# Kernel optimization log

Hardware: AMD Instinct MI355X
Metric: run time of the kernel (lower is better)

## Reference

```python
import jax, jax.numpy as jnp
import numpy as np

B, C, H, W = 8, 512, 64, 64
NH, D = 8, 64            # num_heads, head_dim (C = NH*D)
WH, WW = 8, 8            # window size
EPS = 1e-5
SCALE = D ** -0.5


def _layernorm(x, g, b):
    mu = jnp.mean(x, axis=-1, keepdims=True)
    var = jnp.mean((x - mu) ** 2, axis=-1, keepdims=True)
    return (x - mu) * jax.lax.rsqrt(var + EPS) * g + b


def _rope_cache(n, d):
    pos = jnp.arange(n, dtype=jnp.float32)
    inv_freq = 1.0 / (10000.0 ** (jnp.arange(0, d, 2, dtype=jnp.float32) / d))
    sinusoid = pos[:, None] * inv_freq[None, :]          # (n, d//2)
    return jnp.stack([jnp.sin(sinusoid), jnp.cos(sinusoid)], axis=-1).reshape(n, d)


def _apply_rope(x, rope):
    # x: (B, nH, N, d); rope: (N, d) packed [sin, cos] interleaved
    b, nh, n, d = x.shape
    x_ = x.reshape(b, nh, n, d // 2, 2)
    r = rope.reshape(n, d // 2, 2)
    sin, cos = r[..., 0], r[..., 1]                      # (N, d//2)
    x0, x1 = x_[..., 0], x_[..., 1]
    xr0 = x0 * cos - x1 * sin
    xr1 = x0 * sin + x1 * cos
    return jnp.stack([xr0, xr1], axis=-1).reshape(b, nh, n, d)


def _relative_index(wh, ww):
    ch, cw = np.meshgrid(np.arange(wh), np.arange(ww), indexing='ij')
    flat = np.stack([ch.reshape(-1), cw.reshape(-1)])    # (2, Ws)
    rel = flat[:, :, None] - flat[:, None, :]            # (2, Ws, Ws)
    rel = rel.transpose(1, 2, 0).astype(np.int64)
    rel[..., 0] += wh - 1
    rel[..., 1] += ww - 1
    rel[..., 0] *= 2 * ww - 1
    return jnp.asarray(rel.sum(-1))                      # (Ws, Ws)


def setup_inputs() -> dict:
    key = jax.random.key(0)
    ks = jax.random.split(key, 12)
    s = 0.02
    table_size = (2 * WH - 1) * (2 * WW - 1)
    return {
        'q':  jax.random.normal(ks[0], (B, C, H, W), jnp.float32),
        'kv': jax.random.normal(ks[1], (B, C, H, W), jnp.float32),
        'g_q':  jnp.ones((C,), jnp.float32),  'b_q_ln':  jnp.zeros((C,), jnp.float32),
        'g_kv': jnp.ones((C,), jnp.float32),  'b_kv_ln': jnp.zeros((C,), jnp.float32),
        'Wq': jax.random.normal(ks[2], (C, C), jnp.float32) * s, 'bq': jnp.zeros((C,), jnp.float32),
        'Wk': jax.random.normal(ks[3], (C, C), jnp.float32) * s, 'bk': jnp.zeros((C,), jnp.float32),
        'Wv': jax.random.normal(ks[4], (C, C), jnp.float32) * s, 'bv': jnp.zeros((C,), jnp.float32),
        'Wo': jax.random.normal(ks[5], (C, C), jnp.float32) * s, 'bo': jnp.zeros((C,), jnp.float32),
        'bias_table': jax.random.normal(ks[6], (table_size, NH), jnp.float32) * s,
    }


def reference(q, kv, g_q, b_q_ln, g_kv, b_kv_ln, Wq, bq, Wk, bk, Wv, bv, Wo, bo, bias_table):
    N = H * W
    Hn, Wn = H // WH, W // WW
    nw = Hn * Wn
    Ws = WH * WW

    # flatten NCHW -> (B, N, C)
    q_seq = q.reshape(B, C, N).transpose(0, 2, 1)
    kv_seq = kv.reshape(B, C, N).transpose(0, 2, 1)
    q_seq = _layernorm(q_seq, g_q, b_q_ln)
    kv_seq = _layernorm(kv_seq, g_kv, b_kv_ln)

    Q = (q_seq @ Wq.T + bq).reshape(B, N, NH, D).transpose(0, 2, 1, 3)   # (B,nH,N,d)
    K = (kv_seq @ Wk.T + bk).reshape(B, N, NH, D).transpose(0, 2, 1, 3)
    V = (kv_seq @ Wv.T + bv).reshape(B, N, NH, D).transpose(0, 2, 1, 3)

    rope = _rope_cache(N, D)
    Q = _apply_rope(Q, rope)
    K = _apply_rope(K, rope)

    # window partition: (B,nH,H,W,d) -> (nH, B*nw, Ws, d); head-major to match torch cat order
    def part(x):
        x = x.reshape(B, NH, Hn, WH, Wn, WW, D)
        return x.transpose(1, 0, 2, 4, 3, 5, 6).reshape(NH, B * nw, Ws, D)

    Qw, Kw, Vw = part(Q), part(K), part(V)

    attn = jnp.einsum('hnqd,hnkd->hnqk', Qw, Kw) * SCALE                 # (nH, B*nw, Ws, Ws)
    rel_idx = _relative_index(WH, WW)
    bias = bias_table[rel_idx.reshape(-1)].reshape(Ws, Ws, NH).transpose(2, 0, 1)  # (nH, Ws, Ws)
    attn = attn + bias[:, None, :, :]
    attn = jax.nn.softmax(attn, axis=-1)
    out_w = jnp.einsum('hnqk,hnkd->hnqd', attn, Vw)                      # (nH, B*nw, Ws, d)

    # window reverse + head concat -> (B, N, C)
    out = out_w.reshape(NH, B, Hn, Wn, WH, WW, D)
    out = out.transpose(1, 2, 4, 3, 5, 0, 6).reshape(B, N, NH * D)

    out = out @ Wo.T + bo
    out = out + q_seq                                                    # residual w/ normed q (as in source)
    return out.transpose(0, 2, 1).reshape(B, C, H, W)
```

## Files before the change

### kernel.cpp

```cpp
#include <hip/hip_runtime.h>


typedef unsigned short u16;
typedef __bf16 bf16x8 __attribute__((ext_vector_type(8)));
typedef float f32x4 __attribute__((ext_vector_type(4)));
typedef u16 u16x8 __attribute__((ext_vector_type(8)));

__device__ __forceinline__ u16 f2bf(float f) {
    __bf16 h = (__bf16)f;
    return __builtin_bit_cast(u16, h);
}
__device__ __forceinline__ float bf2f(u16 u) {
    return (float)__builtin_bit_cast(__bf16, u);
}
__device__ __forceinline__ f32x4 mfma16(bf16x8 a, bf16x8 b, f32x4 c) {
    return __builtin_amdgcn_mfma_f32_16x16x32_bf16(a, b, c, 0, 0, 0);
}

__global__ __launch_bounds__(256) void setup_kernel(
    const float* __restrict__ Wq, const float* __restrict__ Wk,
    const float* __restrict__ Wv, const float* __restrict__ Wo,
    const float* __restrict__ btab,
    u16* __restrict__ wq, u16* __restrict__ wk,
    u16* __restrict__ wv, u16* __restrict__ wo,
    float* __restrict__ rope, float* __restrict__ biasf)
{
    int idx = blockIdx.x * 256 + threadIdx.x;
    {
        int w = idx >> 18, e = idx & 262143;
        const float* src = (w == 0) ? Wq : (w == 1) ? Wk : (w == 2) ? Wv : Wo;
        u16* dst = (w == 0) ? wq : (w == 1) ? wk : (w == 2) ? wv : wo;
        dst[e] = f2bf(src[e]);
    }
    if (idx < 131072) {
        int n = idx >> 5, j = idx & 31;
        float inv = powf(10000.0f, -(float)j / 32.0f);
        float a = (float)n * inv;
        float s, c;
        sincosf(a, &s, &c);
        rope[n * 64 + 2 * j] = s;
        rope[n * 64 + 2 * j + 1] = c;
    }
    if (idx < 32768) {
        int q = idx & 63, pp = (idx >> 6) & 63, h = idx >> 12;
        int r1 = pp >> 3, c1 = pp & 7, r2 = q >> 3, c2 = q & 7;
        int ri = (r1 - r2 + 7) * 15 + (c1 - c2 + 7);
        biasf[idx] = btab[ri * 8 + h];
    }
}

__global__ __launch_bounds__(256) void ln_kernel(
    const float* __restrict__ x, const float* __restrict__ g,
    const float* __restrict__ be, u16* __restrict__ out)
{
    __shared__ u16 sX[512 * 36];
    __shared__ float sSum[256];
    __shared__ float sSq[256];
    __shared__ float sMu[32], sInv[32];

    const int tid = threadIdx.x;
    const int b = blockIdx.x >> 7, grp = blockIdx.x & 127;
    const int nbase = grp << 5;
    const int no = tid & 31, cg = tid >> 5;

    const float* xp = x + ((size_t)b << 21) + nbase + no;
    float sum = 0.f, sq = 0.f;
#pragma unroll 4
    for (int i = 0; i < 64; i++) {
        int c = (i << 3) + cg;
        float v = xp[(size_t)c << 12];
        sum += v;
        sq += v * v;
        sX[c * 36 + no] = f2bf(v);
    }
    sSum[tid] = sum;
    sSq[tid] = sq;
    __syncthreads();
    if (tid < 32) {
        float s = 0.f, q = 0.f;
#pragma unroll
        for (int k = 0; k < 8; k++) { s += sSum[k * 32 + tid]; q += sSq[k * 32 + tid]; }
        float mu = s * (1.f / 512.f);
        float var = q * (1.f / 512.f) - mu * mu;
        sMu[tid] = mu;
        sInv[tid] = rsqrtf(var + 1e-5f);
    }
    __syncthreads();

    const int t = tid & 31;
    const int chalf = (tid >> 5) << 3;
    float mu = sMu[t], inv = sInv[t];
    size_t orow = ((size_t)((b << 12) + nbase + t)) * 512;
#pragma unroll
    for (int it = 0; it < 8; it++) {
        int c0 = chalf + (it << 6);
        f32x4 g0 = *(const f32x4*)&g[c0];
        f32x4 g1 = *(const f32x4*)&g[c0 + 4];
        f32x4 e0 = *(const f32x4*)&be[c0];
        f32x4 e1 = *(const f32x4*)&be[c0 + 4];
        u16x8 o;
#pragma unroll
        for (int k = 0; k < 8; k++) {
            float v = bf2f(sX[(c0 + k) * 36 + t]);
            float gg = (k < 4) ? g0[k] : g1[k - 4];
            float bb = (k < 4) ? e0[k] : e1[k - 4];
            o[k] = f2bf((v - mu) * inv * gg + bb);
        }
        *(u16x8*)&out[orow + c0] = o;
    }
}

template <bool ROPE>
__global__ __launch_bounds__(256) void gemm_proj(
    const u16* __restrict__ A, const u16* __restrict__ Bw,
    const float* __restrict__ bias, const float* __restrict__ rope,
    u16* __restrict__ Out)
{
    __shared__ u16 sA[128 * 40];
    __shared__ u16 sB[128 * 40];
    __shared__ u16 sC[64 * 136];

    const int m0 = blockIdx.x * 128;
    const int n0 = blockIdx.y * 128;
    const int tid = threadIdx.x;
    const int lane = tid & 63, wave = tid >> 6;
    const int ln = lane & 15, lq = lane >> 4;
    const int wm = wave & 1, wn = wave >> 1;

    f32x4 acc[4][4] = {};

    for (int kt = 0; kt < 512; kt += 32) {
        __syncthreads();
#pragma unroll
        for (int ps = 0; ps < 2; ps++) {
            int idx = (ps << 8) + tid;
            int row = idx >> 2, seg = idx & 3;
            *(u16x8*)&sA[row * 40 + seg * 8] =
                *(const u16x8*)&A[(size_t)(m0 + row) * 512 + kt + seg * 8];
            *(u16x8*)&sB[row * 40 + seg * 8] =
                *(const u16x8*)&Bw[(size_t)(n0 + row) * 512 + kt + seg * 8];
        }
        __syncthreads();
        bf16x8 af[4], bfr[4];
#pragma unroll
        for (int i = 0; i < 4; i++)
            af[i] = *(const bf16x8*)&sA[(wm * 64 + i * 16 + ln) * 40 + lq * 8];
#pragma unroll
        for (int j = 0; j < 4; j++)
            bfr[j] = *(const bf16x8*)&sB[(wn * 64 + j * 16 + ln) * 40 + lq * 8];
#pragma unroll
        for (int i = 0; i < 4; i++)
#pragma unroll
            for (int j = 0; j < 4; j++)
                acc[i][j] = mfma16(af[i], bfr[j], acc[i][j]);
    }

    float bj[4];
#pragma unroll
    for (int j = 0; j < 4; j++) bj[j] = bias[n0 + wn * 64 + j * 16 + ln];

#pragma unroll
    for (int half = 0; half < 2; half++) {
        __syncthreads();
        if (wm == half) {
#pragma unroll
            for (int i = 0; i < 4; i++)
#pragma unroll
                for (int j = 0; j < 4; j++)
#pragma unroll
                    for (int r = 0; r < 4; r++)
                        sC[(i * 16 + lq * 4 + r) * 136 + wn * 64 + j * 16 + ln] =
                            f2bf(acc[i][j][r] + bj[j]);
        }
        __syncthreads();
#pragma unroll
        for (int it = 0; it < 4; it++) {
            int idx = it * 256 + tid;
            int row = idx >> 4;
            int cseg = (idx & 15) * 8;
            u16x8 v = *(const u16x8*)&sC[row * 136 + cseg];
            int t = m0 + half * 64 + row;
            float f[8];
#pragma unroll
            for (int k = 0; k < 8; k++) f[k] = bf2f(v[k]);
            if (ROPE) {
                int n = t & 4095;
                int d0 = cseg & 63;
                const float* rp = &rope[n * 64 + d0];
                f32x4 r0 = *(const f32x4*)rp;
                f32x4 r1 = *(const f32x4*)(rp + 4);
#pragma unroll
                for (int p = 0; p < 4; p++) {
                    float sn = (p < 2) ? r0[2 * p] : r1[2 * (p - 2)];
                    float cs = (p < 2) ? r0[2 * p + 1] : r1[2 * (p - 2) + 1];
                    float x0 = f[2 * p], x1 = f[2 * p + 1];
                    f[2 * p] = x0 * cs - x1 * sn;
                    f[2 * p + 1] = x0 * sn + x1 * cs;
                }
            }
            u16x8 o;
#pragma unroll
            for (int k = 0; k < 8; k++) o[k] = f2bf(f[k]);
            *(u16x8*)&Out[(size_t)t * 512 + n0 + cseg] = o;
        }
    }
}

__global__ __launch_bounds__(256) void gemm_out(
    const u16* __restrict__ A, const u16* __restrict__ Bw,
    const float* __restrict__ bias, const u16* __restrict__ qn,
    float* __restrict__ Out)
{
    __shared__ u16 sA[128 * 40];
    __shared__ u16 sB[128 * 40];

    const int m0 = blockIdx.x * 128;
    const int n0 = blockIdx.y * 128;
    const int tid = threadIdx.x;
    const int lane = tid & 63, wave = tid >> 6;
    const int ln = lane & 15, lq = lane >> 4;
    const int wm = wave & 1, wn = wave >> 1;

    f32x4 acc[4][4] = {};

    for (int kt = 0; kt < 512; kt += 32) {
        __syncthreads();
#pragma unroll
        for (int ps = 0; ps < 2; ps++) {
            int idx = (ps << 8) + tid;
            int row = idx >> 2, seg = idx & 3;
            *(u16x8*)&sA[row * 40 + seg * 8] =
                *(const u16x8*)&A[(size_t)(m0 + row) * 512 + kt + seg * 8];
            *(u16x8*)&sB[row * 40 + seg * 8] =
                *(const u16x8*)&Bw[(size_t)(n0 + row) * 512 + kt + seg * 8];
        }
        __syncthreads();
        bf16x8 af[4], bfr[4];
#pragma unroll
        for (int i = 0; i < 4; i++)
            af[i] = *(const bf16x8*)&sA[(wm * 64 + i * 16 + ln) * 40 + lq * 8];
#pragma unroll
        for (int j = 0; j < 4; j++)
            bfr[j] = *(const bf16x8*)&sB[(wn * 64 + j * 16 + ln) * 40 + lq * 8];
#pragma unroll
        for (int i = 0; i < 4; i++)
#pragma unroll
            for (int j = 0; j < 4; j++)
                acc[i][j] = mfma16(af[i], bfr[j], acc[i][j]);
    }

    int cj[4];
    float bj[4];
#pragma unroll
    for (int j = 0; j < 4; j++) {
        cj[j] = n0 + wn * 64 + j * 16 + ln;
        bj[j] = bias[cj[j]];
    }
#pragma unroll
    for (int i = 0; i < 4; i++) {
        int t0 = m0 + wm * 64 + i * 16 + lq * 4;
        int bb = t0 >> 12, nn = t0 & 4095;
#pragma unroll
        for (int j = 0; j < 4; j++) {
            f32x4 v;
#pragma unroll
            for (int r = 0; r < 4; r++)
                v[r] = acc[i][j][r] + bj[j] + bf2f(qn[(size_t)(t0 + r) * 512 + cj[j]]);
            *(f32x4*)&Out[((size_t)((bb << 9) + cj[j]) << 12) + nn] = v;
        }
    }
}

__global__ __launch_bounds__(256) void attn_kernel(
    const u16* __restrict__ Q, const u16* __restrict__ K, const u16* __restrict__ V,
    const float* __restrict__ biasf, u16* __restrict__ Out)
{
    __shared__ u16 sQ[64 * 72];
    __shared__ u16 sK[64 * 72];
    __shared__ u16 sVT[64 * 72];
    __shared__ u16 sP[4][16 * 72];

    const int tid = threadIdx.x;
    const int h = blockIdx.x & 7;
    const int g = blockIdx.x >> 3;
    const int b = g >> 6, wi = g & 63;
    const int hn = wi >> 3, wn = wi & 7;
    const int nwbase = (b << 12) + (hn << 3) * 64 + (wn << 3);

    const int lane = tid & 63, wave = tid >> 6;
    const int ln = lane & 15, lq = lane >> 4;

    {
        int p = tid >> 2, seg = tid & 3;
        int t = nwbase + ((p >> 3) << 6) + (p & 7);
        size_t base = (size_t)t * 512 + h * 64 + seg * 16;
        u16x8 q0 = *(const u16x8*)&Q[base];
        u16x8 q1 = *(const u16x8*)&Q[base + 8];
        *(u16x8*)&sQ[p * 72 + seg * 16] = q0;
        *(u16x8*)&sQ[p * 72 + seg * 16 + 8] = q1;
        u16x8 k0 = *(const u16x8*)&K[base];
        u16x8 k1 = *(const u16x8*)&K[base + 8];
        *(u16x8*)&sK[p * 72 + seg * 16] = k0;
        *(u16x8*)&sK[p * 72 + seg * 16 + 8] = k1;
        u16x8 v0 = *(const u16x8*)&V[base];
        u16x8 v1 = *(const u16x8*)&V[base + 8];
#pragma unroll
        for (int k = 0; k < 8; k++) {
            sVT[(seg * 16 + k) * 72 + p] = v0[k];
            sVT[(seg * 16 + 8 + k) * 72 + p] = v1[k];
        }
    }
    __syncthreads();

    f32x4 s[4] = {};
#pragma unroll
    for (int ks = 0; ks < 2; ks++) {
        bf16x8 a = *(const bf16x8*)&sQ[(wave * 16 + ln) * 72 + ks * 32 + lq * 8];
#pragma unroll
        for (int j = 0; j < 4; j++) {
            bf16x8 bb = *(const bf16x8*)&sK[(j * 16 + ln) * 72 + ks * 32 + lq * 8];
            s[j] = mfma16(a, bb, s[j]);
        }
    }

    float sv[4][4];
#pragma unroll
    for (int r = 0; r < 4; r++) {
        const float* bp = &biasf[((h * 64 + wave * 16 + lq * 4 + r) << 6) + ln];
#pragma unroll
        for (int j = 0; j < 4; j++) sv[r][j] = s[j][r] * 0.125f + bp[j * 16];
    }
#pragma unroll
    for (int r = 0; r < 4; r++) {
        float m = fmaxf(fmaxf(sv[r][0], sv[r][1]), fmaxf(sv[r][2], sv[r][3]));
        m = fmaxf(m, __shfl_xor(m, 1));
        m = fmaxf(m, __shfl_xor(m, 2));
        m = fmaxf(m, __shfl_xor(m, 4));
        m = fmaxf(m, __shfl_xor(m, 8));
        float sum = 0.f;
#pragma unroll
        for (int j = 0; j < 4; j++) {
            sv[r][j] = __expf(sv[r][j] - m);
            sum += sv[r][j];
        }
        sum += __shfl_xor(sum, 1);
        sum += __shfl_xor(sum, 2);
        sum += __shfl_xor(sum, 4);
        sum += __shfl_xor(sum, 8);
        float rinv = 1.f / sum;
#pragma unroll
        for (int j = 0; j < 4; j++)
            sP[wave][(lq * 4 + r) * 72 + j * 16 + ln] = f2bf(sv[r][j] * rinv);
    }

    f32x4 o[4] = {};
#pragma unroll
    for (int ks = 0; ks < 2; ks++) {
        bf16x8 a = *(const bf16x8*)&sP[wave][ln * 72 + ks * 32 + lq * 8];
#pragma unroll
        for (int jd = 0; jd < 4; jd++) {
            bf16x8 bb = *(const bf16x8*)&sVT[(jd * 16 + ln) * 72 + ks * 32 + lq * 8];
            o[jd] = mfma16(a, bb, o[jd]);
        }
    }

#pragma unroll
    for (int r = 0; r < 4; r++) {
        int p = wave * 16 + lq * 4 + r;
        int t = nwbase + ((p >> 3) << 6) + (p & 7);
        size_t base = (size_t)t * 512 + h * 64 + ln;
#pragma unroll
        for (int jd = 0; jd < 4; jd++) Out[base + jd * 16] = f2bf(o[jd][r]);
    }
}

extern "C" void kernel_launch(void* const* d_in, const int* in_sizes, int n_in,
                              void* d_out, int out_size, void* d_ws, size_t ws_size,
                              hipStream_t stream)
{
    const float* q    = (const float*)d_in[0];
    const float* kv   = (const float*)d_in[1];
    const float* g_q  = (const float*)d_in[2];
    const float* b_q  = (const float*)d_in[3];
    const float* g_kv = (const float*)d_in[4];
    const float* b_kv = (const float*)d_in[5];
    const float* Wq   = (const float*)d_in[6];
    const float* bq   = (const float*)d_in[7];
    const float* Wk   = (const float*)d_in[8];
    const float* bk   = (const float*)d_in[9];
    const float* Wv   = (const float*)d_in[10];
    const float* bv   = (const float*)d_in[11];
    const float* Wo   = (const float*)d_in[12];
    const float* bo   = (const float*)d_in[13];
    const float* btab = (const float*)d_in[14];

    char* ws = (char*)d_ws;
    u16* qn      = (u16*)(ws);
    u16* kvn     = (u16*)(ws + 33554432);
    u16* Vv      = (u16*)(ws + 67108864);
    float* rope  = (float*)(ws + 100663296);
    float* biasf = (float*)(ws + 101711872);
    u16* wq      = (u16*)(ws + 101842944);
    u16* wk      = (u16*)(ws + 102367232);
    u16* wv      = (u16*)(ws + 102891520);
    u16* wo      = (u16*)(ws + 103415808);
    u16* aout    = kvn;
    u16* Qr      = (u16*)d_out;
    u16* Kr      = Qr + 16777216;

    setup_kernel<<<4096, 256, 0, stream>>>(Wq, Wk, Wv, Wo, btab, wq, wk, wv, wo, rope, biasf);
    ln_kernel<<<1024, 256, 0, stream>>>(q, g_q, b_q, qn);
    ln_kernel<<<1024, 256, 0, stream>>>(kv, g_kv, b_kv, kvn);
    gemm_proj<true><<<dim3(256, 4), 256, 0, stream>>>(qn, wq, bq, rope, Qr);
    gemm_proj<true><<<dim3(256, 4), 256, 0, stream>>>(kvn, wk, bk, rope, Kr);
    gemm_proj<false><<<dim3(256, 4), 256, 0, stream>>>(kvn, wv, bv, rope, Vv);
    attn_kernel<<<4096, 256, 0, stream>>>(Qr, Kr, Vv, biasf, aout);
    gemm_out<<<dim3(256, 4), 256, 0, stream>>>(aout, wo, bo, qn, (float*)d_out);
}
```

Baseline: 383.5 us.

## Store Q/K/V in window-major order, transpose V in GEMM, use direct global-to-LDS loads

Q and K projection outputs are written in a window-permuted token order (bit swap of token index), and a new V GEMM writes V transposed per head. This lets the attention kernel load contiguous 64-token tiles and skip its scattered gather and LDS transpose. The output GEMM reads and writes through the same permutation. All GEMMs now stage tiles with global_load_lds into unpadded LDS, and the LayerNorm store path is remapped with a smaller LDS pitch. The unpadded 32-element LDS rows may add bank conflicts on the fragment reads.

```diff
diff --git a/kernel.cpp b/kernel.cpp
--- a/kernel.cpp
+++ b/kernel.cpp
@@ -5,6 +5,7 @@
 typedef __bf16 bf16x8 __attribute__((ext_vector_type(8)));
 typedef float f32x4 __attribute__((ext_vector_type(4)));
 typedef u16 u16x8 __attribute__((ext_vector_type(8)));
+typedef u16 u16x4 __attribute__((ext_vector_type(4)));
 
 __device__ __forceinline__ u16 f2bf(float f) {
     __bf16 h = (__bf16)f;
@@ -15,6 +16,13 @@
 }
 __device__ __forceinline__ f32x4 mfma16(bf16x8 a, bf16x8 b, f32x4 c) {
     return __builtin_amdgcn_mfma_f32_16x16x32_bf16(a, b, c, 0, 0, 0);
+}
+__device__ __forceinline__ void gl_lds16(const u16* g, u16* l) {
+    __builtin_amdgcn_global_load_lds((const __attribute__((address_space(1))) void*)g,
+                                     (__attribute__((address_space(3))) void*)l, 16, 0, 0);
+}
+__device__ __forceinline__ int swapb(int n) {
+    return (n & 0xE07) | ((n & 0x1C0) >> 3) | ((n & 0x038) << 3);
 }
 
 __global__ __launch_bounds__(256) void setup_kernel(
@@ -53,7 +61,7 @@
     const float* __restrict__ x, const float* __restrict__ g,
     const float* __restrict__ be, u16* __restrict__ out)
 {
-    __shared__ u16 sX[512 * 36];
+    __shared__ u16 sX[512 * 33];
     __shared__ float sSum[256];
     __shared__ float sSq[256];
     __shared__ float sMu[32], sInv[32];
@@ -71,7 +79,7 @@
         float v = xp[(size_t)c << 12];
         sum += v;
         sq += v * v;
-        sX[c * 36 + no] = f2bf(v);
+        sX[c * 33 + no] = f2bf(v);
     }
     sSum[tid] = sum;
     sSq[tid] = sq;
@@ -87,13 +95,13 @@
     }
     __syncthreads();
 
-    const int t = tid & 31;
-    const int chalf = (tid >> 5) << 3;
+    const int t = tid >> 3;
+    const int cs = (tid & 7) << 3;
     float mu = sMu[t], inv = sInv[t];
     size_t orow = ((size_t)((b << 12) + nbase + t)) * 512;
 #pragma unroll
     for (int it = 0; it < 8; it++) {
-        int c0 = chalf + (it << 6);
+        int c0 = cs + (it << 6);
         f32x4 g0 = *(const f32x4*)&g[c0];
         f32x4 g1 = *(const f32x4*)&g[c0 + 4];
         f32x4 e0 = *(const f32x4*)&be[c0];
@@ -101,7 +109,7 @@
         u16x8 o;
 #pragma unroll
         for (int k = 0; k < 8; k++) {
-            float v = bf2f(sX[(c0 + k) * 36 + t]);
+            float v = bf2f(sX[(c0 + k) * 33 + t]);
             float gg = (k < 4) ? g0[k] : g1[k - 4];
             float bb = (k < 4) ? e0[k] : e1[k - 4];
             o[k] = f2bf((v - mu) * inv * gg + bb);
@@ -116,8 +124,8 @@
     const float* __restrict__ bias, const float* __restrict__ rope,
     u16* __restrict__ Out)
 {
-    __shared__ u16 sA[128 * 40];
-    __shared__ u16 sB[128 * 40];
+    __shared__ u16 sA[128 * 32];
+    __shared__ u16 sB[128 * 32];
     __shared__ u16 sC[64 * 136];
 
     const int m0 = blockIdx.x * 128;
@@ -127,32 +135,38 @@
     const int ln = lane & 15, lq = lane >> 4;
     const int wm = wave & 1, wn = wave >> 1;
 
+    const int srow = wave * 16 + (lane >> 2);
+    const int sseg = (lane & 3) << 3;
+    const u16* gA0 = A + (size_t)(m0 + srow) * 512 + sseg;
+    const u16* gA1 = gA0 + (size_t)64 * 512;
+    const u16* gB0 = Bw + (size_t)(n0 + srow) * 512 + sseg;
+    const u16* gB1 = gB0 + (size_t)64 * 512;
+    u16* lA0 = &sA[wave * 16 * 32];
+    u16* lA1 = &sA[(64 + wave * 16) * 32];
+    u16* lB0 = &sB[wave * 16 * 32];
+    u16* lB1 = &sB[(64 + wave * 16) * 32];
+
     f32x4 acc[4][4] = {};
 
     for (int kt = 0; kt < 512; kt += 32) {
-        __syncthreads();
-#pragma unroll
-        for (int ps = 0; ps < 2; ps++) {
-            int idx = (ps << 8) + tid;
-            int row = idx >> 2, seg = idx & 3;
-            *(u16x8*)&sA[row * 40 + seg * 8] =
-                *(const u16x8*)&A[(size_t)(m0 + row) * 512 + kt + seg * 8];
-            *(u16x8*)&sB[row * 40 + seg * 8] =
-                *(const u16x8*)&Bw[(size_t)(n0 + row) * 512 + kt + seg * 8];
-        }
+        gl_lds16(gA0 + kt, lA0);
+        gl_lds16(gA1 + kt, lA1);
+        gl_lds16(gB0 + kt, lB0);
+        gl_lds16(gB1 + kt, lB1);
         __syncthreads();
         bf16x8 af[4], bfr[4];
 #pragma unroll
         for (int i = 0; i < 4; i++)
-            af[i] = *(const bf16x8*)&sA[(wm * 64 + i * 16 + ln) * 40 + lq * 8];
+            af[i] = *(const bf16x8*)&sA[(wm * 64 + i * 16 + ln) * 32 + lq * 8];
 #pragma unroll
         for (int j = 0; j < 4; j++)
-            bfr[j] = *(const bf16x8*)&sB[(wn * 64 + j * 16 + ln) * 40 + lq * 8];
+            bfr[j] = *(const bf16x8*)&sB[(wn * 64 + j * 16 + ln) * 32 + lq * 8];
 #pragma unroll
         for (int i = 0; i < 4; i++)
 #pragma unroll
             for (int j = 0; j < 4; j++)
                 acc[i][j] = mfma16(af[i], bfr[j], acc[i][j]);
+        __syncthreads();
     }
 
     float bj[4];
@@ -180,11 +194,11 @@
             int cseg = (idx & 15) * 8;
             u16x8 v = *(const u16x8*)&sC[row * 136 + cseg];
             int t = m0 + half * 64 + row;
+            int n = t & 4095, bb = t >> 12;
             float f[8];
 #pragma unroll
             for (int k = 0; k < 8; k++) f[k] = bf2f(v[k]);
             if (ROPE) {
-                int n = t & 4095;
                 int d0 = cseg & 63;
                 const float* rp = &rope[n * 64 + d0];
                 f32x4 r0 = *(const f32x4*)rp;
@@ -201,18 +215,19 @@
             u16x8 o;
 #pragma unroll
             for (int k = 0; k < 8; k++) o[k] = f2bf(f[k]);
-            *(u16x8*)&Out[(size_t)t * 512 + n0 + cseg] = o;
-        }
-    }
-}
-
-__global__ __launch_bounds__(256) void gemm_out(
+            int wp = swapb(n);
+            *(u16x8*)&Out[(size_t)((bb << 12) + wp) * 512 + n0 + cseg] = o;
+        }
+    }
+}
+
+__global__ __launch_bounds__(256) void gemm_v(
     const u16* __restrict__ A, const u16* __restrict__ Bw,
-    const float* __restrict__ bias, const u16* __restrict__ qn,
-    float* __restrict__ Out)
-{
-    __shared__ u16 sA[128 * 40];
-    __shared__ u16 sB[128 * 40];
+    const float* __restrict__ bias, u16* __restrict__ VT)
+{
+    __shared__ u16 sA[128 * 32];
+    __shared__ u16 sB[128 * 32];
+    __shared__ u16 sCv[128 * 72];
 
     const int m0 = blockIdx.x * 128;
     const int n0 = blockIdx.y * 128;
@@ -221,32 +236,124 @@
     const int ln = lane & 15, lq = lane >> 4;
     const int wm = wave & 1, wn = wave >> 1;
 
+    const int wq0 = m0 & 4095;
+    const int bhi = m0 & ~4095;
+    const int bb = m0 >> 12;
+
+    const int srow = wave * 16 + (lane >> 2);
+    const int sseg = (lane & 3) << 3;
+    const int nA0 = swapb(wq0 + srow);
+    const int nA1 = swapb(wq0 + 64 + srow);
+    const u16* gA0 = A + (size_t)(bhi + nA0) * 512 + sseg;
+    const u16* gA1 = A + (size_t)(bhi + nA1) * 512 + sseg;
+    const u16* gB0 = Bw + (size_t)(n0 + srow) * 512 + sseg;
+    const u16* gB1 = gB0 + (size_t)64 * 512;
+    u16* lA0 = &sA[wave * 16 * 32];
+    u16* lA1 = &sA[(64 + wave * 16) * 32];
+    u16* lB0 = &sB[wave * 16 * 32];
+    u16* lB1 = &sB[(64 + wave * 16) * 32];
+
     f32x4 acc[4][4] = {};
 
     for (int kt = 0; kt < 512; kt += 32) {
-        __syncthreads();
-#pragma unroll
-        for (int ps = 0; ps < 2; ps++) {
-            int idx = (ps << 8) + tid;
-            int row = idx >> 2, seg = idx & 3;
-            *(u16x8*)&sA[row * 40 + seg * 8] =
-                *(const u16x8*)&A[(size_t)(m0 + row) * 512 + kt + seg * 8];
-            *(u16x8*)&sB[row * 40 + seg * 8] =
-                *(const u16x8*)&Bw[(size_t)(n0 + row) * 512 + kt + seg * 8];
-        }
+        gl_lds16(gA0 + kt, lA0);
+        gl_lds16(gA1 + kt, lA1);
+        gl_lds16(gB0 + kt, lB0);
+        gl_lds16(gB1 + kt, lB1);
         __syncthreads();
         bf16x8 af[4], bfr[4];
 #pragma unroll
         for (int i = 0; i < 4; i++)
-            af[i] = *(const bf16x8*)&sA[(wm * 64 + i * 16 + ln) * 40 + lq * 8];
+            af[i] = *(const bf16x8*)&sA[(wm * 64 + i * 16 + ln) * 32 + lq * 8];
 #pragma unroll
         for (int j = 0; j < 4; j++)
-            bfr[j] = *(const bf16x8*)&sB[(wn * 64 + j * 16 + ln) * 40 + lq * 8];
+            bfr[j] = *(const bf16x8*)&sB[(wn * 64 + j * 16 + ln) * 32 + lq * 8];
 #pragma unroll
         for (int i = 0; i < 4; i++)
 #pragma unroll
             for (int j = 0; j < 4; j++)
                 acc[i][j] = mfma16(af[i], bfr[j], acc[i][j]);
+        __syncthreads();
+    }
+
+    float bj[4];
+#pragma unroll
+    for (int j = 0; j < 4; j++) bj[j] = bias[n0 + wn * 64 + j * 16 + ln];
+
+#pragma unroll
+    for (int half = 0; half < 2; half++) {
+        __syncthreads();
+        if (wm == half) {
+#pragma unroll
+            for (int i = 0; i < 4; i++)
+#pragma unroll
+                for (int j = 0; j < 4; j++) {
+                    u16x4 pk;
+#pragma unroll
+                    for (int r = 0; r < 4; r++) pk[r] = f2bf(acc[i][j][r] + bj[j]);
+                    *(u16x4*)&sCv[(wn * 64 + j * 16 + ln) * 72 + i * 16 + lq * 4] = pk;
+                }
+        }
+        __syncthreads();
+#pragma unroll
+        for (int ii = 0; ii < 4; ii++) {
+            int idx = ii * 256 + tid;
+            int col = idx >> 3, ch = (idx & 7) << 3;
+            u16x8 v = *(const u16x8*)&sCv[col * 72 + ch];
+            int c = n0 + col;
+            int hh = c >> 6, dd = c & 63;
+            *(u16x8*)&VT[((size_t)((((bb << 3) + hh) << 6) + dd)) * 4096 + wq0 + half * 64 + ch] = v;
+        }
+    }
+}
+
+__global__ __launch_bounds__(256) void gemm_out(
+    const u16* __restrict__ A, const u16* __restrict__ Bw,
+    const float* __restrict__ bias, const u16* __restrict__ qn,
+    float* __restrict__ Out)
+{
+    __shared__ u16 sA[128 * 32];
+    __shared__ u16 sB[128 * 32];
+
+    const int m0 = blockIdx.x * 128;
+    const int n0 = blockIdx.y * 128;
+    const int tid = threadIdx.x;
+    const int lane = tid & 63, wave = tid >> 6;
+    const int ln = lane & 15, lq = lane >> 4;
+    const int wm = wave & 1, wn = wave >> 1;
+
+    const int srow = wave * 16 + (lane >> 2);
+    const int sseg = (lane & 3) << 3;
+    const u16* gA0 = A + (size_t)(m0 + srow) * 512 + sseg;
+    const u16* gA1 = gA0 + (size_t)64 * 512;
+    const u16* gB0 = Bw + (size_t)(n0 + srow) * 512 + sseg;
+    const u16* gB1 = gB0 + (size_t)64 * 512;
+    u16* lA0 = &sA[wave * 16 * 32];
+    u16* lA1 = &sA[(64 + wave * 16) * 32];
+    u16* lB0 = &sB[wave * 16 * 32];
+    u16* lB1 = &sB[(64 + wave * 16) * 32];
+
+    f32x4 acc[4][4] = {};
+
+    for (int kt = 0; kt < 512; kt += 32) {
+        gl_lds16(gA0 + kt, lA0);
+        gl_lds16(gA1 + kt, lA1);
+        gl_lds16(gB0 + kt, lB0);
+        gl_lds16(gB1 + kt, lB1);
+        __syncthreads();
+        bf16x8 af[4], bfr[4];
+#pragma unroll
+        for (int i = 0; i < 4; i++)
+            af[i] = *(const bf16x8*)&sA[(wm * 64 + i * 16 + ln) * 32 + lq * 8];
+#pragma unroll
+        for (int j = 0; j < 4; j++)
+            bfr[j] = *(const bf16x8*)&sB[(wn * 64 + j * 16 + ln) * 32 + lq * 8];
+#pragma unroll
+        for (int i = 0; i < 4; i++)
+#pragma unroll
+            for (int j = 0; j < 4; j++)
+                acc[i][j] = mfma16(af[i], bfr[j], acc[i][j]);
+        __syncthreads();
     }
 
     int cj[4];
@@ -259,20 +366,22 @@
 #pragma unroll
     for (int i = 0; i < 4; i++) {
         int t0 = m0 + wm * 64 + i * 16 + lq * 4;
-        int bb = t0 >> 12, nn = t0 & 4095;
+        int bb = t0 >> 12;
+        int nb = swapb(t0 & 4095);
 #pragma unroll
         for (int j = 0; j < 4; j++) {
             f32x4 v;
 #pragma unroll
             for (int r = 0; r < 4; r++)
-                v[r] = acc[i][j][r] + bj[j] + bf2f(qn[(size_t)(t0 + r) * 512 + cj[j]]);
-            *(f32x4*)&Out[((size_t)((bb << 9) + cj[j]) << 12) + nn] = v;
+                v[r] = acc[i][j][r] + bj[j] +
+                       bf2f(qn[((size_t)(bb << 12) + nb + r) * 512 + cj[j]]);
+            *(f32x4*)&Out[((size_t)((bb << 9) + cj[j]) << 12) + nb] = v;
         }
     }
 }
 
 __global__ __launch_bounds__(256) void attn_kernel(
-    const u16* __restrict__ Q, const u16* __restrict__ K, const u16* __restrict__ V,
+    const u16* __restrict__ Q, const u16* __restrict__ K, const u16* __restrict__ VT,
     const float* __restrict__ biasf, u16* __restrict__ Out)
 {
     __shared__ u16 sQ[64 * 72];
@@ -282,33 +391,22 @@
 
     const int tid = threadIdx.x;
     const int h = blockIdx.x & 7;
-    const int g = blockIdx.x >> 3;
-    const int b = g >> 6, wi = g & 63;
-    const int hn = wi >> 3, wn = wi & 7;
-    const int nwbase = (b << 12) + (hn << 3) * 64 + (wn << 3);
-
+    const int w = (blockIdx.x >> 3) & 63;
+    const int b = blockIdx.x >> 9;
     const int lane = tid & 63, wave = tid >> 6;
     const int ln = lane & 15, lq = lane >> 4;
 
-    {
-        int p = tid >> 2, seg = tid & 3;
-        int t = nwbase + ((p >> 3) << 6) + (p & 7);
-        size_t base = (size_t)t * 512 + h * 64 + seg * 16;
-        u16x8 q0 = *(const u16x8*)&Q[base];
-        u16x8 q1 = *(const u16x8*)&Q[base + 8];
-        *(u16x8*)&sQ[p * 72 + seg * 16] = q0;
-        *(u16x8*)&sQ[p * 72 + seg * 16 + 8] = q1;
-        u16x8 k0 = *(const u16x8*)&K[base];
-        u16x8 k1 = *(const u16x8*)&K[base + 8];
-        *(u16x8*)&sK[p * 72 + seg * 16] = k0;
-        *(u16x8*)&sK[p * 72 + seg * 16 + 8] = k1;
-        u16x8 v0 = *(const u16x8*)&V[base];
-        u16x8 v1 = *(const u16x8*)&V[base + 8];
-#pragma unroll
-        for (int k = 0; k < 8; k++) {
-            sVT[(seg * 16 + k) * 72 + p] = v0[k];
-            sVT[(seg * 16 + 8 + k) * 72 + p] = v1[k];
-        }
+    const size_t qrow0 = (size_t)(b << 12) + w * 64;
+    const size_t vrow0 = ((size_t)(((b << 3) + h) << 6)) * 4096 + w * 64;
+
+#pragma unroll
+    for (int ii = 0; ii < 2; ii++) {
+        int idx = ii * 256 + tid;
+        int row = idx >> 3, ch = (idx & 7) << 3;
+        size_t ga = (qrow0 + row) * 512 + h * 64 + ch;
+        *(u16x8*)&sQ[row * 72 + ch] = *(const u16x8*)&Q[ga];
+        *(u16x8*)&sK[row * 72 + ch] = *(const u16x8*)&K[ga];
+        *(u16x8*)&sVT[row * 72 + ch] = *(const u16x8*)&VT[vrow0 + (size_t)row * 4096 + ch];
     }
     __syncthreads();
 
@@ -365,12 +463,16 @@
     }
 
 #pragma unroll
-    for (int r = 0; r < 4; r++) {
-        int p = wave * 16 + lq * 4 + r;
-        int t = nwbase + ((p >> 3) << 6) + (p & 7);
-        size_t base = (size_t)t * 512 + h * 64 + ln;
-#pragma unroll
-        for (int jd = 0; jd < 4; jd++) Out[base + jd * 16] = f2bf(o[jd][r]);
+    for (int r = 0; r < 4; r++)
+#pragma unroll
+        for (int jd = 0; jd < 4; jd++)
+            sQ[(wave * 16 + lq * 4 + r) * 72 + jd * 16 + ln] = f2bf(o[jd][r]);
+    __syncthreads();
+#pragma unroll
+    for (int ii = 0; ii < 2; ii++) {
+        int idx = ii * 256 + tid;
+        int row = idx >> 3, ch = (idx & 7) << 3;
+        *(u16x8*)&Out[(qrow0 + row) * 512 + h * 64 + ch] = *(const u16x8*)&sQ[row * 72 + ch];
     }
 }
 
@@ -397,7 +499,7 @@
     char* ws = (char*)d_ws;
     u16* qn      = (u16*)(ws);
     u16* kvn     = (u16*)(ws + 33554432);
-    u16* Vv      = (u16*)(ws + 67108864);
+    u16* VT      = (u16*)(ws + 67108864);
     float* rope  = (float*)(ws + 100663296);
     float* biasf = (float*)(ws + 101711872);
     u16* wq      = (u16*)(ws + 101842944);
@@ -413,7 +515,7 @@
     ln_kernel<<<1024, 256, 0, stream>>>(kv, g_kv, b_kv, kvn);
     gemm_proj<true><<<dim3(256, 4), 256, 0, stream>>>(qn, wq, bq, rope, Qr);
     gemm_proj<true><<<dim3(256, 4), 256, 0, stream>>>(kvn, wk, bk, rope, Kr);
-    gemm_proj<false><<<dim3(256, 4), 256, 0, stream>>>(kvn, wv, bv, rope, Vv);
-    attn_kernel<<<4096, 256, 0, stream>>>(Qr, Kr, Vv, biasf, aout);
+    gemm_v<<<dim3(256, 4), 256, 0, stream>>>(kvn, wv, bv, VT);
+    attn_kernel<<<4096, 256, 0, stream>>>(Qr, Kr, VT, biasf, aout);
     gemm_out<<<dim3(256, 4), 256, 0, stream>>>(aout, wo, bo, qn, (float*)d_out);
 }
```

Measured after the change: 365.6 us. 1.05x faster.
